# Kernel optimization log

Measured on AMD Instinct MI355X. Metric: run time of the kernel, lower is better.

The kernel has to match this reference:

```python
import jax, jax.numpy as jnp
import numpy as np

B, S, D, F, E, K = 4, 2048, 512, 1024, 8, 2

def setup_inputs() -> dict:
    key = jax.random.key(0)
    ks = jax.random.split(key, 7)
    hidden = jax.random.normal(ks[0], (B, S, D), dtype=jnp.float32)
    top_k_indices = jax.random.randint(ks[1], (B, S, K), 0, E, dtype=jnp.int32)
    top_k_weights = jax.random.uniform(ks[2], (B, S, K), dtype=jnp.float32)
    scale1 = 1.0 / np.sqrt(D)
    scale2 = 1.0 / np.sqrt(F)
    W1 = jax.random.normal(ks[3], (E, D, F), dtype=jnp.float32) * scale1
    b1 = jnp.zeros((E, F), dtype=jnp.float32)
    W2 = jax.random.normal(ks[4], (E, F, D), dtype=jnp.float32) * scale2
    b2 = jnp.zeros((E, D), dtype=jnp.float32)
    return {"hidden": hidden, "top_k_indices": top_k_indices,
            "top_k_weights": top_k_weights, "W1": W1, "b1": b1, "W2": W2, "b2": b2}

def reference(hidden, top_k_indices, top_k_weights, W1, b1, W2, b2):
    b, s, d = hidden.shape
    e = W1.shape[0]
    x = hidden.reshape(-1, d)                      # [T, D]
    idx = top_k_indices.reshape(-1, top_k_indices.shape[-1])   # [T, K]
    w = top_k_weights.reshape(-1, top_k_weights.shape[-1])     # [T, K]
    # combine weight per (token, expert): sum over k slots routed to expert e
    onehot = jax.nn.one_hot(idx, e, dtype=w.dtype)             # [T, K, E]
    cw = jnp.einsum('tk,tke->et', w, onehot)                   # [E, T]
    def step(acc, params):
        W1e, b1e, W2e, b2e, cwe = params
        h = jax.nn.gelu(x @ W1e + b1e)                         # [T, F]
        y = h @ W2e + b2e                                      # [T, D]
        return acc + cwe[:, None] * y, None
    out, _ = jax.lax.scan(step, jnp.zeros_like(x), (W1, b1, W2, b2, cw))
    return out.reshape(b, s, d)
```

## Files before the change

### kernel.cpp

```cpp
#include <hip/hip_runtime.h>
#include <hip/hip_bf16.h>

#define T_TOK 8192
#define DDIM  512
#define FDIM  1024
#define NEXP  8
#define KTOP  2
#define NSLOT (T_TOK * KTOP)
#define MAX_ROWS 17408
#define MAX_T64  272

typedef __attribute__((ext_vector_type(8))) __bf16 bf16x8;
typedef __attribute__((ext_vector_type(4))) __bf16 bf16x4;
typedef __attribute__((ext_vector_type(4))) float  f32x4;

typedef __attribute__((address_space(1))) const unsigned int* gp1;
typedef __attribute__((address_space(3))) unsigned int*       lp3;
#define GL2LDS(g, l) __builtin_amdgcn_global_load_lds((gp1)(const void*)(g), (lp3)(void*)(l), 16, 0, 0)


__device__ __forceinline__ float gelu_tanh(float x){
    float u = 0.7978845608028654f * (x + 0.044715f * x * x * x);
    return 0.5f * x * (1.0f + tanhf(u));
}

__device__ __forceinline__ unsigned short f2bf(float v){
    __hip_bfloat16 b = __float2bfloat16(v);
    return *(unsigned short*)&b;
}

__global__ void cast_x_bf16(const float* __restrict__ src, unsigned short* __restrict__ dst,
                            int n){
    int i = blockIdx.x * blockDim.x + threadIdx.x;
    if (i < n) dst[i] = f2bf(src[i]);
}

__global__ __launch_bounds__(1024) void bucket_kernel(
    const int* __restrict__ idx, int* __restrict__ meta, int2* __restrict__ map,
    int* __restrict__ list, int* __restrict__ slot2row)
{
    __shared__ int scan[NEXP][1024];
    const int tid = threadIdx.x;
    const int base = tid * 16;

    int mye[16];
    int c[NEXP];
    #pragma unroll
    for (int e = 0; e < NEXP; e++) c[e] = 0;
    #pragma unroll
    for (int i = 0; i < 16; i++){
        mye[i] = idx[base + i] & 7;
        c[mye[i]]++;
    }
    #pragma unroll
    for (int e = 0; e < NEXP; e++) scan[e][tid] = c[e];
    __syncthreads();

    for (int off = 1; off < 1024; off <<= 1){
        int t[NEXP];
        #pragma unroll
        for (int e = 0; e < NEXP; e++) t[e] = (tid >= off) ? scan[e][tid - off] : 0;
        __syncthreads();
        #pragma unroll
        for (int e = 0; e < NEXP; e++) scan[e][tid] += t[e];
        __syncthreads();
    }

    int cnt[NEXP], pad[NEXP], off_e[NEXP];
    int o = 0;
    #pragma unroll
    for (int e = 0; e < NEXP; e++){
        cnt[e] = scan[e][1023];
        pad[e] = (cnt[e] + 127) & ~127;
        off_e[e] = o;
        o += pad[e];
    }
    const int nrows = o;

    if (tid == 0){
        int nt = 0;
        for (int e = 0; e < NEXP; e++){
            meta[17 + e] = off_e[e];
            for (int tb = 0; tb < (pad[e] >> 6); tb++)
                map[nt++] = make_int2(e, off_e[e] + tb * 64);
        }
        meta[16] = nt;
    }

    int run[NEXP];
    #pragma unroll
    for (int e = 0; e < NEXP; e++) run[e] = off_e[e] + scan[e][tid] - c[e];
    #pragma unroll
    for (int i = 0; i < 16; i++){
        int e = mye[i];
        int gg = run[e]++;
        list[gg] = (base + i) >> 1;
        slot2row[base + i] = gg;
    }

    for (int p = tid; p < nrows; p += 1024){
        #pragma unroll
        for (int e = 0; e < NEXP; e++){
            if (p >= off_e[e] + cnt[e] && p < off_e[e] + pad[e]) list[p] = 0;
        }
    }
}

__global__ void transpose_cast(const float* __restrict__ src,
                               unsigned short* __restrict__ dst, int R, int C){
    __shared__ unsigned short tile[32][33];
    int e = blockIdx.z;
    int c0 = blockIdx.x * 32, r0 = blockIdx.y * 32;
    int tx = threadIdx.x, ty = threadIdx.y;
    const float* sf = src + (size_t)e * R * C;
    unsigned short* d = dst + (size_t)e * R * C;
    #pragma unroll
    for (int i = 0; i < 4; i++)
        tile[ty + i * 8][tx] = f2bf(sf[(size_t)(r0 + ty + i * 8) * C + c0 + tx]);
    __syncthreads();
    #pragma unroll
    for (int i = 0; i < 4; i++)
        d[(size_t)(c0 + ty + i * 8) * R + r0 + tx] = tile[tx][ty + i * 8];
}

__global__ __launch_bounds__(256, 2) void gemm1_kernel(
    const unsigned short* __restrict__ x,
    const unsigned short* __restrict__ w1t,
    const float* __restrict__ b1,
    const int* __restrict__ meta,
    const int2* __restrict__ map,
    const int* __restrict__ list,
    unsigned short* __restrict__ h)
{
    if ((int)blockIdx.y >= meta[16]) return;
    int2 em = map[blockIdx.y];
    const int e = em.x, grow0 = em.y;
    const int n0 = blockIdx.x * 128;

    __shared__ __align__(16) unsigned short As[64 * 32];
    __shared__ __align__(16) unsigned short Bs[128 * 32];

    const int tid = threadIdx.x;
    const int wave = tid >> 6;
    const int lane = tid & 63;
    const int rA = tid >> 2, kqA = tid & 3;
    const int rB0 = tid >> 2, kqB0 = tid & 3;
    const int rB1 = (tid + 256) >> 2, kqB1 = tid & 3;
    const int tokA = list[grow0 + rA];
    const unsigned short* gA  = x + (size_t)tokA * DDIM + kqA * 8;
    const unsigned short* gB0 = w1t + ((size_t)e * FDIM + n0 + rB0) * DDIM + kqB0 * 8;
    const unsigned short* gB1 = w1t + ((size_t)e * FDIM + n0 + rB1) * DDIM + kqB1 * 8;
    char* lA  = (char*)As + wave * 1024;
    char* lB0 = (char*)Bs + wave * 1024;
    char* lB1 = (char*)Bs + 4096 + wave * 1024;

    const int quad = lane >> 4, lrow = lane & 15;
    const int wn = wave * 32;

    f32x4 acc[4][2];
    #pragma unroll
    for (int i = 0; i < 4; i++){ acc[i][0] = (f32x4)0.0f; acc[i][1] = (f32x4)0.0f; }

    for (int kk = 0; kk < DDIM; kk += 32){
        __syncthreads();
        GL2LDS(gA + kk, lA);
        GL2LDS(gB0 + kk, lB0);
        GL2LDS(gB1 + kk, lB1);
        __syncthreads();
        bf16x8 af[4], bfr[2];
        #pragma unroll
        for (int i = 0; i < 4; i++)
            af[i] = *(const bf16x8*)&As[(i * 16 + lrow) * 32 + quad * 8];
        #pragma unroll
        for (int j = 0; j < 2; j++)
            bfr[j] = *(const bf16x8*)&Bs[(wn + j * 16 + lrow) * 32 + quad * 8];
        #pragma unroll
        for (int i = 0; i < 4; i++)
            #pragma unroll
            for (int j = 0; j < 2; j++)
                acc[i][j] = __builtin_amdgcn_mfma_f32_16x16x32_bf16(af[i], bfr[j], acc[i][j], 0, 0, 0);
    }

    #pragma unroll
    for (int i = 0; i < 4; i++){
        #pragma unroll
        for (int j = 0; j < 2; j++){
            int cn = n0 + wn + j * 16 + lrow;
            float bias = b1[e * FDIM + cn];
            #pragma unroll
            for (int r = 0; r < 4; r++){
                int gr = grow0 + i * 16 + quad * 4 + r;
                h[(size_t)gr * FDIM + cn] = f2bf(gelu_tanh(acc[i][j][r] + bias));
            }
        }
    }
}

__global__ __launch_bounds__(256, 2) void gemm2_kernel(
    const unsigned short* __restrict__ h,
    const unsigned short* __restrict__ w2t,
    const float* __restrict__ b2,
    const int* __restrict__ meta,
    const int2* __restrict__ map,
    unsigned short* __restrict__ y)
{
    if ((int)blockIdx.y >= meta[16]) return;
    int2 em = map[blockIdx.y];
    const int e = em.x, grow0 = em.y;
    const int n0 = blockIdx.x * 128;

    __shared__ __align__(16) unsigned short As[64 * 32];
    __shared__ __align__(16) unsigned short Bs[128 * 32];

    const int tid = threadIdx.x;
    const int wave = tid >> 6;
    const int lane = tid & 63;
    const int rA = tid >> 2, kqA = tid & 3;
    const int rB0 = tid >> 2, kqB0 = tid & 3;
    const int rB1 = (tid + 256) >> 2, kqB1 = tid & 3;
    const unsigned short* gA  = h + (size_t)(grow0 + rA) * FDIM + kqA * 8;
    const unsigned short* gB0 = w2t + ((size_t)e * DDIM + n0 + rB0) * FDIM + kqB0 * 8;
    const unsigned short* gB1 = w2t + ((size_t)e * DDIM + n0 + rB1) * FDIM + kqB1 * 8;
    char* lA  = (char*)As + wave * 1024;
    char* lB0 = (char*)Bs + wave * 1024;
    char* lB1 = (char*)Bs + 4096 + wave * 1024;

    const int quad = lane >> 4, lrow = lane & 15;
    const int wn = wave * 32;

    f32x4 acc[4][2];
    #pragma unroll
    for (int i = 0; i < 4; i++){ acc[i][0] = (f32x4)0.0f; acc[i][1] = (f32x4)0.0f; }

    for (int kk = 0; kk < FDIM; kk += 32){
        __syncthreads();
        GL2LDS(gA + kk, lA);
        GL2LDS(gB0 + kk, lB0);
        GL2LDS(gB1 + kk, lB1);
        __syncthreads();
        bf16x8 af[4], bfr[2];
        #pragma unroll
        for (int i = 0; i < 4; i++)
            af[i] = *(const bf16x8*)&As[(i * 16 + lrow) * 32 + quad * 8];
        #pragma unroll
        for (int j = 0; j < 2; j++)
            bfr[j] = *(const bf16x8*)&Bs[(wn + j * 16 + lrow) * 32 + quad * 8];
        #pragma unroll
        for (int i = 0; i < 4; i++)
            #pragma unroll
            for (int j = 0; j < 2; j++)
                acc[i][j] = __builtin_amdgcn_mfma_f32_16x16x32_bf16(af[i], bfr[j], acc[i][j], 0, 0, 0);
    }

    #pragma unroll
    for (int i = 0; i < 4; i++){
        #pragma unroll
        for (int j = 0; j < 2; j++){
            int cn = n0 + wn + j * 16 + lrow;
            float bias = b2[e * DDIM + cn];
            #pragma unroll
            for (int r = 0; r < 4; r++){
                int gr = grow0 + i * 16 + quad * 4 + r;
                y[(size_t)gr * DDIM + cn] = f2bf(acc[i][j][r] + bias);
            }
        }
    }
}

__global__ void combine_kernel(const unsigned short* __restrict__ y,
                               const int* __restrict__ slot2row,
                               const float* __restrict__ wk,
                               float* __restrict__ out){
    int g = blockIdx.x * blockDim.x + threadIdx.x;
    int t = g >> 7, seg = g & 127;
    int ra = slot2row[2 * t], rb = slot2row[2 * t + 1];
    float wa = wk[2 * t];
    float wb = wk[2 * t + 1];
    bf16x4 ya = *(const bf16x4*)(y + (size_t)ra * DDIM + seg * 4);
    bf16x4 yb = *(const bf16x4*)(y + (size_t)rb * DDIM + seg * 4);
    float4 o;
    o.x = wa * (float)ya[0] + wb * (float)yb[0];
    o.y = wa * (float)ya[1] + wb * (float)yb[1];
    o.z = wa * (float)ya[2] + wb * (float)yb[2];
    o.w = wa * (float)ya[3] + wb * (float)yb[3];
    *(float4*)(out + (size_t)t * DDIM + seg * 4) = o;
}

extern "C" void kernel_launch(void* const* d_in, const int* in_sizes, int n_in,
                              void* d_out, int out_size, void* d_ws, size_t ws_size,
                              hipStream_t stream){
    const float* x   = (const float*)d_in[0];
    const int*   idx = (const int*)d_in[1];
    const float* wk  = (const float*)d_in[2];
    const float* W1  = (const float*)d_in[3];
    const float* b1  = (const float*)d_in[4];
    const float* W2  = (const float*)d_in[5];
    const float* b2  = (const float*)d_in[6];
    float* out = (float*)d_out;

    char* ws = (char*)d_ws;
    int*   meta     = (int*)ws;
    int2*  map      = (int2*)(ws + 512);
    int*   list     = (int*)(ws + 4096);
    int*   slot2row = (int*)(ws + 81920);
    unsigned short* xbf = (unsigned short*)(ws + 262144);
    unsigned short* w1t = (unsigned short*)(ws + 8650752);
    unsigned short* w2t = (unsigned short*)(ws + 17039360);
    unsigned short* h   = (unsigned short*)(ws + 25427968);
    unsigned short* y   = (unsigned short*)(ws + 61079552);
    if (ws_size < 78905344u) return;

    cast_x_bf16<<<(T_TOK * DDIM) / 256, 256, 0, stream>>>(x, xbf, T_TOK * DDIM);

    transpose_cast<<<dim3(FDIM / 32, DDIM / 32, NEXP), dim3(32, 8), 0, stream>>>(
        W1, w1t, DDIM, FDIM);
    transpose_cast<<<dim3(DDIM / 32, FDIM / 32, NEXP), dim3(32, 8), 0, stream>>>(
        W2, w2t, FDIM, DDIM);

    bucket_kernel<<<1, 1024, 0, stream>>>(idx, meta, map, list, slot2row);

    gemm1_kernel<<<dim3(FDIM / 128, MAX_T64), 256, 0, stream>>>(
        xbf, w1t, b1, meta, map, list, h);
    gemm2_kernel<<<dim3(DDIM / 128, MAX_T64), 256, 0, stream>>>(
        h, w2t, b2, meta, map, y);

    combine_kernel<<<(T_TOK * DDIM / 4) / 256, 256, 0, stream>>>(y, slot2row, wk, out);
}
```

Measured before the change: 217.7 us.

## Enlarge expert GEMM tiles to 128x128x64 with XCD-aware block swizzle

Both grouped GEMMs move from 64x128 tiles with K=32 steps to 128x128 tiles with K=64 steps. Each wave now computes a 64x64 sub-tile, which raises MFMA work per LDS load and halves the number of barriers. Workgroup ids are remapped so consecutive tiles land on the same XCD for better L2 reuse, and routing tiles are padded to 128 rows. The tanh GELU is replaced by an equivalent exp-based form, and the x cast is vectorised to 8 elements per thread. In exchange the kernels use more LDS and registers per block, which may lower occupancy.

```diff
diff --git a/kernel.cpp b/kernel.cpp
--- a/kernel.cpp
+++ b/kernel.cpp
@@ -8,20 +8,21 @@
 #define KTOP  2
 #define NSLOT (T_TOK * KTOP)
 #define MAX_ROWS 17408
-#define MAX_T64  272
+#define MAX_T128 136
 
 typedef __attribute__((ext_vector_type(8))) __bf16 bf16x8;
 typedef __attribute__((ext_vector_type(4))) __bf16 bf16x4;
 typedef __attribute__((ext_vector_type(4))) float  f32x4;
+typedef __attribute__((ext_vector_type(8))) unsigned short u16x8;
 
 typedef __attribute__((address_space(1))) const unsigned int* gp1;
 typedef __attribute__((address_space(3))) unsigned int*       lp3;
 #define GL2LDS(g, l) __builtin_amdgcn_global_load_lds((gp1)(const void*)(g), (lp3)(void*)(l), 16, 0, 0)
 
 
-__device__ __forceinline__ float gelu_tanh(float x){
+__device__ __forceinline__ float gelu_fast(float x){
     float u = 0.7978845608028654f * (x + 0.044715f * x * x * x);
-    return 0.5f * x * (1.0f + tanhf(u));
+    return x / (1.0f + __expf(-2.0f * u));
 }
 
 __device__ __forceinline__ unsigned short f2bf(float v){
@@ -30,9 +31,16 @@
 }
 
 __global__ void cast_x_bf16(const float* __restrict__ src, unsigned short* __restrict__ dst,
-                            int n){
+                            int n8){
     int i = blockIdx.x * blockDim.x + threadIdx.x;
-    if (i < n) dst[i] = f2bf(src[i]);
+    if (i >= n8) return;
+    const float4* s = (const float4*)src;
+    float4 a = s[2 * i];
+    float4 b = s[2 * i + 1];
+    u16x8 o;
+    o[0] = f2bf(a.x); o[1] = f2bf(a.y); o[2] = f2bf(a.z); o[3] = f2bf(a.w);
+    o[4] = f2bf(b.x); o[5] = f2bf(b.y); o[6] = f2bf(b.z); o[7] = f2bf(b.w);
+    *(u16x8*)(dst + (size_t)i * 8) = o;
 }
 
 __global__ __launch_bounds__(1024) void bucket_kernel(
@@ -81,8 +89,8 @@
         int nt = 0;
         for (int e = 0; e < NEXP; e++){
             meta[17 + e] = off_e[e];
-            for (int tb = 0; tb < (pad[e] >> 6); tb++)
-                map[nt++] = make_int2(e, off_e[e] + tb * 64);
+            for (int tb = 0; tb < (pad[e] >> 7); tb++)
+                map[nt++] = make_int2(e, off_e[e] + tb * 128);
         }
         meta[16] = nt;
     }
@@ -132,65 +140,95 @@
     const int* __restrict__ list,
     unsigned short* __restrict__ h)
 {
-    if ((int)blockIdx.y >= meta[16]) return;
-    int2 em = map[blockIdx.y];
+    const int ntiles = meta[16];
+    const int nwg = ntiles * (FDIM / 128);
+    int id = blockIdx.y * gridDim.x + blockIdx.x;
+    if (id >= nwg) return;
+    int q = nwg >> 3, r = nwg & 7;
+    int xcd = id & 7, rank = id >> 3;
+    int swz = (xcd < r) ? (xcd * (q + 1) + rank)
+                        : (r * (q + 1) + (xcd - r) * q + rank);
+    const int tile = swz >> 3;
+    const int n0 = (swz & 7) * 128;
+    int2 em = map[tile];
     const int e = em.x, grow0 = em.y;
-    const int n0 = blockIdx.x * 128;
-
-    __shared__ __align__(16) unsigned short As[64 * 32];
-    __shared__ __align__(16) unsigned short Bs[128 * 32];
-
-    const int tid = threadIdx.x;
+
+    __shared__ __align__(16) unsigned short As[128 * 64];
+    __shared__ __align__(16) unsigned short Bs[128 * 64];
+
+    const int tid  = threadIdx.x;
     const int wave = tid >> 6;
     const int lane = tid & 63;
-    const int rA = tid >> 2, kqA = tid & 3;
-    const int rB0 = tid >> 2, kqB0 = tid & 3;
-    const int rB1 = (tid + 256) >> 2, kqB1 = tid & 3;
-    const int tokA = list[grow0 + rA];
-    const unsigned short* gA  = x + (size_t)tokA * DDIM + kqA * 8;
-    const unsigned short* gB0 = w1t + ((size_t)e * FDIM + n0 + rB0) * DDIM + kqB0 * 8;
-    const unsigned short* gB1 = w1t + ((size_t)e * FDIM + n0 + rB1) * DDIM + kqB1 * 8;
-    char* lA  = (char*)As + wave * 1024;
-    char* lB0 = (char*)Bs + wave * 1024;
-    char* lB1 = (char*)Bs + 4096 + wave * 1024;
+    const int ko   = lane & 7;
+    const int rsub = lane >> 3;
+
+    const unsigned short* gA0; const unsigned short* gA1;
+    const unsigned short* gA2; const unsigned short* gA3;
+    const unsigned short* gB0; const unsigned short* gB1;
+    const unsigned short* gB2; const unsigned short* gB3;
+    {
+        int r0_ = 0 * 32 + wave * 8 + rsub;
+        int r1_ = 1 * 32 + wave * 8 + rsub;
+        int r2_ = 2 * 32 + wave * 8 + rsub;
+        int r3_ = 3 * 32 + wave * 8 + rsub;
+        gA0 = x + (size_t)list[grow0 + r0_] * DDIM + ko * 8;
+        gA1 = x + (size_t)list[grow0 + r1_] * DDIM + ko * 8;
+        gA2 = x + (size_t)list[grow0 + r2_] * DDIM + ko * 8;
+        gA3 = x + (size_t)list[grow0 + r3_] * DDIM + ko * 8;
+        gB0 = w1t + ((size_t)e * FDIM + n0 + r0_) * DDIM + ko * 8;
+        gB1 = w1t + ((size_t)e * FDIM + n0 + r1_) * DDIM + ko * 8;
+        gB2 = w1t + ((size_t)e * FDIM + n0 + r2_) * DDIM + ko * 8;
+        gB3 = w1t + ((size_t)e * FDIM + n0 + r3_) * DDIM + ko * 8;
+    }
+    char* lA = (char*)As + wave * 1024;
+    char* lB = (char*)Bs + wave * 1024;
 
     const int quad = lane >> 4, lrow = lane & 15;
-    const int wn = wave * 32;
-
-    f32x4 acc[4][2];
-    #pragma unroll
-    for (int i = 0; i < 4; i++){ acc[i][0] = (f32x4)0.0f; acc[i][1] = (f32x4)0.0f; }
-
-    for (int kk = 0; kk < DDIM; kk += 32){
-        __syncthreads();
-        GL2LDS(gA + kk, lA);
-        GL2LDS(gB0 + kk, lB0);
-        GL2LDS(gB1 + kk, lB1);
-        __syncthreads();
-        bf16x8 af[4], bfr[2];
-        #pragma unroll
-        for (int i = 0; i < 4; i++)
-            af[i] = *(const bf16x8*)&As[(i * 16 + lrow) * 32 + quad * 8];
-        #pragma unroll
-        for (int j = 0; j < 2; j++)
-            bfr[j] = *(const bf16x8*)&Bs[(wn + j * 16 + lrow) * 32 + quad * 8];
-        #pragma unroll
-        for (int i = 0; i < 4; i++)
-            #pragma unroll
-            for (int j = 0; j < 2; j++)
-                acc[i][j] = __builtin_amdgcn_mfma_f32_16x16x32_bf16(af[i], bfr[j], acc[i][j], 0, 0, 0);
-    }
-
-    #pragma unroll
-    for (int i = 0; i < 4; i++){
-        #pragma unroll
-        for (int j = 0; j < 2; j++){
-            int cn = n0 + wn + j * 16 + lrow;
-            float bias = b1[e * FDIM + cn];
-            #pragma unroll
-            for (int r = 0; r < 4; r++){
-                int gr = grow0 + i * 16 + quad * 4 + r;
-                h[(size_t)gr * FDIM + cn] = f2bf(gelu_tanh(acc[i][j][r] + bias));
+    const int wr = (wave >> 1) * 64;
+    const int wc = (wave & 1) * 64;
+
+    f32x4 acc[4][4];
+    #pragma unroll
+    for (int i = 0; i < 4; i++)
+        #pragma unroll
+        for (int j = 0; j < 4; j++) acc[i][j] = (f32x4)0.0f;
+
+    for (int kk = 0; kk < DDIM; kk += 64){
+        __syncthreads();
+        GL2LDS(gA0 + kk, lA);          GL2LDS(gB0 + kk, lB);
+        GL2LDS(gA1 + kk, lA + 4096);   GL2LDS(gB1 + kk, lB + 4096);
+        GL2LDS(gA2 + kk, lA + 8192);   GL2LDS(gB2 + kk, lB + 8192);
+        GL2LDS(gA3 + kk, lA + 12288);  GL2LDS(gB3 + kk, lB + 12288);
+        __syncthreads();
+        bf16x8 a[4][2], b[4][2];
+        #pragma unroll
+        for (int i = 0; i < 4; i++){
+            #pragma unroll
+            for (int ks = 0; ks < 2; ks++){
+                a[i][ks] = *(const bf16x8*)&As[(wr + i * 16 + lrow) * 64 + ks * 32 + quad * 8];
+                b[i][ks] = *(const bf16x8*)&Bs[(wc + i * 16 + lrow) * 64 + ks * 32 + quad * 8];
+            }
+        }
+        #pragma unroll
+        for (int i = 0; i < 4; i++){
+            #pragma unroll
+            for (int j = 0; j < 4; j++){
+                acc[i][j] = __builtin_amdgcn_mfma_f32_16x16x32_bf16(a[i][0], b[j][0], acc[i][j], 0, 0, 0);
+                acc[i][j] = __builtin_amdgcn_mfma_f32_16x16x32_bf16(a[i][1], b[j][1], acc[i][j], 0, 0, 0);
+            }
+        }
+    }
+
+    #pragma unroll
+    for (int j = 0; j < 4; j++){
+        int cn = n0 + wc + j * 16 + lrow;
+        float bias = b1[e * FDIM + cn];
+        #pragma unroll
+        for (int i = 0; i < 4; i++){
+            #pragma unroll
+            for (int rr = 0; rr < 4; rr++){
+                int gr = grow0 + wr + i * 16 + quad * 4 + rr;
+                h[(size_t)gr * FDIM + cn] = f2bf(gelu_fast(acc[i][j][rr] + bias));
             }
         }
     }
@@ -204,64 +242,95 @@
     const int2* __restrict__ map,
     unsigned short* __restrict__ y)
 {
-    if ((int)blockIdx.y >= meta[16]) return;
-    int2 em = map[blockIdx.y];
+    const int ntiles = meta[16];
+    const int nwg = ntiles * (DDIM / 128);
+    int id = blockIdx.y * gridDim.x + blockIdx.x;
+    if (id >= nwg) return;
+    int q = nwg >> 3, r = nwg & 7;
+    int xcd = id & 7, rank = id >> 3;
+    int swz = (xcd < r) ? (xcd * (q + 1) + rank)
+                        : (r * (q + 1) + (xcd - r) * q + rank);
+    const int tile = swz >> 2;
+    const int n0 = (swz & 3) * 128;
+    int2 em = map[tile];
     const int e = em.x, grow0 = em.y;
-    const int n0 = blockIdx.x * 128;
-
-    __shared__ __align__(16) unsigned short As[64 * 32];
-    __shared__ __align__(16) unsigned short Bs[128 * 32];
-
-    const int tid = threadIdx.x;
+
+    __shared__ __align__(16) unsigned short As[128 * 64];
+    __shared__ __align__(16) unsigned short Bs[128 * 64];
+
+    const int tid  = threadIdx.x;
     const int wave = tid >> 6;
     const int lane = tid & 63;
-    const int rA = tid >> 2, kqA = tid & 3;
-    const int rB0 = tid >> 2, kqB0 = tid & 3;
-    const int rB1 = (tid + 256) >> 2, kqB1 = tid & 3;
-    const unsigned short* gA  = h + (size_t)(grow0 + rA) * FDIM + kqA * 8;
-    const unsigned short* gB0 = w2t + ((size_t)e * DDIM + n0 + rB0) * FDIM + kqB0 * 8;
-    const unsigned short* gB1 = w2t + ((size_t)e * DDIM + n0 + rB1) * FDIM + kqB1 * 8;
-    char* lA  = (char*)As + wave * 1024;
-    char* lB0 = (char*)Bs + wave * 1024;
-    char* lB1 = (char*)Bs + 4096 + wave * 1024;
+    const int ko   = lane & 7;
+    const int rsub = lane >> 3;
+
+    const unsigned short* gA0; const unsigned short* gA1;
+    const unsigned short* gA2; const unsigned short* gA3;
+    const unsigned short* gB0; const unsigned short* gB1;
+    const unsigned short* gB2; const unsigned short* gB3;
+    {
+        int r0_ = 0 * 32 + wave * 8 + rsub;
+        int r1_ = 1 * 32 + wave * 8 + rsub;
+        int r2_ = 2 * 32 + wave * 8 + rsub;
+        int r3_ = 3 * 32 + wave * 8 + rsub;
+        gA0 = h + (size_t)(grow0 + r0_) * FDIM + ko * 8;
+        gA1 = h + (size_t)(grow0 + r1_) * FDIM + ko * 8;
+        gA2 = h + (size_t)(grow0 + r2_) * FDIM + ko * 8;
+        gA3 = h + (size_t)(grow0 + r3_) * FDIM + ko * 8;
+        gB0 = w2t + ((size_t)e * DDIM + n0 + r0_) * FDIM + ko * 8;
+        gB1 = w2t + ((size_t)e * DDIM + n0 + r1_) * FDIM + ko * 8;
+        gB2 = w2t + ((size_t)e * DDIM + n0 + r2_) * FDIM + ko * 8;
+        gB3 = w2t + ((size_t)e * DDIM + n0 + r3_) * FDIM + ko * 8;
+    }
+    char* lA = (char*)As + wave * 1024;
+    char* lB = (char*)Bs + wave * 1024;
 
     const int quad = lane >> 4, lrow = lane & 15;
-    const int wn = wave * 32;
-
-    f32x4 acc[4][2];
-    #pragma unroll
-    for (int i = 0; i < 4; i++){ acc[i][0] = (f32x4)0.0f; acc[i][1] = (f32x4)0.0f; }
-
-    for (int kk = 0; kk < FDIM; kk += 32){
-        __syncthreads();
-        GL2LDS(gA + kk, lA);
-        GL2LDS(gB0 + kk, lB0);
-        GL2LDS(gB1 + kk, lB1);
-        __syncthreads();
-        bf16x8 af[4], bfr[2];
-        #pragma unroll
-        for (int i = 0; i < 4; i++)
-            af[i] = *(const bf16x8*)&As[(i * 16 + lrow) * 32 + quad * 8];
-        #pragma unroll
-        for (int j = 0; j < 2; j++)
-            bfr[j] = *(const bf16x8*)&Bs[(wn + j * 16 + lrow) * 32 + quad * 8];
-        #pragma unroll
-        for (int i = 0; i < 4; i++)
-            #pragma unroll
-            for (int j = 0; j < 2; j++)
-                acc[i][j] = __builtin_amdgcn_mfma_f32_16x16x32_bf16(af[i], bfr[j], acc[i][j], 0, 0, 0);
-    }
-
-    #pragma unroll
-    for (int i = 0; i < 4; i++){
-        #pragma unroll
-        for (int j = 0; j < 2; j++){
-            int cn = n0 + wn + j * 16 + lrow;
-            float bias = b2[e * DDIM + cn];
-            #pragma unroll
-            for (int r = 0; r < 4; r++){
-                int gr = grow0 + i * 16 + quad * 4 + r;
-                y[(size_t)gr * DDIM + cn] = f2bf(acc[i][j][r] + bias);
+    const int wr = (wave >> 1) * 64;
+    const int wc = (wave & 1) * 64;
+
+    f32x4 acc[4][4];
+    #pragma unroll
+    for (int i = 0; i < 4; i++)
+        #pragma unroll
+        for (int j = 0; j < 4; j++) acc[i][j] = (f32x4)0.0f;
+
+    for (int kk = 0; kk < FDIM; kk += 64){
+        __syncthreads();
+        GL2LDS(gA0 + kk, lA);          GL2LDS(gB0 + kk, lB);
+        GL2LDS(gA1 + kk, lA + 4096);   GL2LDS(gB1 + kk, lB + 4096);
+        GL2LDS(gA2 + kk, lA + 8192);   GL2LDS(gB2 + kk, lB + 8192);
+        GL2LDS(gA3 + kk, lA + 12288);  GL2LDS(gB3 + kk, lB + 12288);
+        __syncthreads();
+        bf16x8 a[4][2], b[4][2];
+        #pragma unroll
+        for (int i = 0; i < 4; i++){
+            #pragma unroll
+            for (int ks = 0; ks < 2; ks++){
+                a[i][ks] = *(const bf16x8*)&As[(wr + i * 16 + lrow) * 64 + ks * 32 + quad * 8];
+                b[i][ks] = *(const bf16x8*)&Bs[(wc + i * 16 + lrow) * 64 + ks * 32 + quad * 8];
+            }
+        }
+        #pragma unroll
+        for (int i = 0; i < 4; i++){
+            #pragma unroll
+            for (int j = 0; j < 4; j++){
+                acc[i][j] = __builtin_amdgcn_mfma_f32_16x16x32_bf16(a[i][0], b[j][0], acc[i][j], 0, 0, 0);
+                acc[i][j] = __builtin_amdgcn_mfma_f32_16x16x32_bf16(a[i][1], b[j][1], acc[i][j], 0, 0, 0);
+            }
+        }
+    }
+
+    #pragma unroll
+    for (int j = 0; j < 4; j++){
+        int cn = n0 + wc + j * 16 + lrow;
+        float bias = b2[e * DDIM + cn];
+        #pragma unroll
+        for (int i = 0; i < 4; i++){
+            #pragma unroll
+            for (int rr = 0; rr < 4; rr++){
+                int gr = grow0 + wr + i * 16 + quad * 4 + rr;
+                y[(size_t)gr * DDIM + cn] = f2bf(acc[i][j][rr] + bias);
             }
         }
     }
@@ -310,7 +379,7 @@
     unsigned short* y   = (unsigned short*)(ws + 61079552);
     if (ws_size < 78905344u) return;
 
-    cast_x_bf16<<<(T_TOK * DDIM) / 256, 256, 0, stream>>>(x, xbf, T_TOK * DDIM);
+    cast_x_bf16<<<(T_TOK * DDIM / 8) / 256, 256, 0, stream>>>(x, xbf, T_TOK * DDIM / 8);
 
     transpose_cast<<<dim3(FDIM / 32, DDIM / 32, NEXP), dim3(32, 8), 0, stream>>>(
         W1, w1t, DDIM, FDIM);
@@ -319,9 +388,9 @@
 
     bucket_kernel<<<1, 1024, 0, stream>>>(idx, meta, map, list, slot2row);
 
-    gemm1_kernel<<<dim3(FDIM / 128, MAX_T64), 256, 0, stream>>>(
+    gemm1_kernel<<<dim3(FDIM / 128, MAX_T128), 256, 0, stream>>>(
         xbf, w1t, b1, meta, map, list, h);
-    gemm2_kernel<<<dim3(DDIM / 128, MAX_T64), 256, 0, stream>>>(
+    gemm2_kernel<<<dim3(DDIM / 128, MAX_T128), 256, 0, stream>>>(
         h, w2t, b2, meta, map, y);
 
     combine_kernel<<<(T_TOK * DDIM / 4) / 256, 256, 0, stream>>>(y, slot2row, wk, out);
```

After: 197.9 us. 9.1% less time.
